# Performance work log

Measured on AMD Instinct MI355X. Metric: run time of the kernel, lower is better.

## Reference

```python
import jax, jax.numpy as jnp
import numpy as np

G = 512  # number of graphs per batch


def gcn_conv(x, edge_index, edge_attr, W):
    # x:[N,Fin], edge_index:[2,E], edge_attr:[E,1], W:[Fin,Fout]
    n = x.shape[0]
    loop = jnp.arange(n)
    row = jnp.concatenate([edge_index[0], loop])
    col = jnp.concatenate([edge_index[1], loop])
    w = jnp.concatenate([edge_attr[:, 0], jnp.ones((n,), x.dtype)])
    deg = jnp.zeros((n,), x.dtype).at[col].add(jnp.ones_like(w))
    dinv = jnp.clip(deg, 1e-12) ** -0.5
    norm = dinv[row] * w * dinv[col]
    h = x @ W  # [N,Fout]
    msg = h[row] * norm[:, None]  # [E+N,Fout] gather+scale
    return jnp.zeros_like(h).at[col].add(msg)  # scatter-add


def mean_pool(x, batch):
    s = jnp.zeros((G, x.shape[1]), x.dtype).at[batch].add(x)
    c = jnp.zeros((G,), x.dtype).at[batch].add(1.0)
    return s / jnp.clip(c, 1.0)[:, None]


def setup_inputs() -> dict:
    key = jax.random.key(0)
    ks = jax.random.split(key, 32)
    Nd, Ed, Np, Ep = 100000, 500000, 200000, 2000000
    d = {
        "drug_x": jax.random.normal(ks[0], (Nd, 78), jnp.float32),
        "drug_edge_index": jax.random.randint(ks[1], (2, Ed), 0, Nd),
        "drug_edge_attr": jax.random.uniform(ks[2], (Ed, 1), jnp.float32),
        "drug_batch": jnp.sort(jax.random.randint(ks[3], (Nd,), 0, G)),
        "protein_x": jax.random.normal(ks[4], (Np, 20), jnp.float32),
        "protein_edge_index": jax.random.randint(ks[5], (2, Ep), 0, Np),
        "protein_edge_attr": jax.random.uniform(ks[6], (Ep, 1), jnp.float32),
        "protein_batch": jnp.sort(jax.random.randint(ks[7], (Np,), 0, G)),
    }
    def w(k, i, o):
        return jax.random.normal(k, (i, o), jnp.float32) / np.sqrt(i)
    d.update({
        "dW1": w(ks[8], 78, 78), "dW2": w(ks[9], 78, 156), "dW3": w(ks[10], 156, 312),
        "dL1_w": w(ks[11], 312, 1024), "dL1_b": jnp.zeros((1024,), jnp.float32),
        "dL2_w": w(ks[12], 1024, 64), "dL2_b": jnp.zeros((64,), jnp.float32),
        "pW1": w(ks[13], 20, 20), "pW2": w(ks[14], 20, 40), "pW3": w(ks[15], 40, 80),
        "pL1_w": w(ks[16], 80, 1024), "pL1_b": jnp.zeros((1024,), jnp.float32),
        "pL2_w": w(ks[17], 1024, 64), "pL2_b": jnp.zeros((64,), jnp.float32),
        "fW1": w(ks[18], 128, 1024), "fb1": jnp.zeros((1024,), jnp.float32),
        "fW2": w(ks[19], 1024, 512), "fb2": jnp.zeros((512,), jnp.float32),
        "fW3": w(ks[20], 512, 1), "fb3": jnp.zeros((1,), jnp.float32),
    })
    return d


def reference(drug_x, drug_edge_index, drug_edge_attr, drug_batch,
              protein_x, protein_edge_index, protein_edge_attr, protein_batch,
              dW1, dW2, dW3, dL1_w, dL1_b, dL2_w, dL2_b,
              pW1, pW2, pW3, pL1_w, pL1_b, pL2_w, pL2_b,
              fW1, fb1, fW2, fb2, fW3, fb3):
    relu = jax.nn.relu
    x = relu(gcn_conv(drug_x, drug_edge_index, drug_edge_attr, dW1))
    x = relu(gcn_conv(x, drug_edge_index, drug_edge_attr, dW2))
    x = relu(gcn_conv(x, drug_edge_index, drug_edge_attr, dW3))
    x = mean_pool(x, drug_batch)
    x = relu(x @ dL1_w + dL1_b)
    x = relu(x @ dL2_w + dL2_b)
    p = relu(gcn_conv(protein_x, protein_edge_index, protein_edge_attr, pW1))
    p = relu(gcn_conv(p, protein_edge_index, protein_edge_attr, pW2))
    p = relu(gcn_conv(p, protein_edge_index, protein_edge_attr, pW3))
    p = mean_pool(p, protein_batch)
    p = relu(p @ pL1_w + pL1_b)
    p = relu(p @ pL2_w + pL2_b)
    c = jnp.concatenate([x, p], axis=1)  # [G,128]
    h = relu(c @ fW1 + fb1)
    h = relu(h @ fW2 + fb2)
    out = h @ fW3 + fb3  # [G,1]
    return out[:, 0]
```

## Files before the change

### kernel.cpp

```cpp
#include <hip/hip_runtime.h>
#include <math.h>

#define NGRAPH 512

typedef __attribute__((ext_vector_type(8))) __bf16 bf16x8;
typedef __attribute__((ext_vector_type(4))) float f32x4;

__device__ __forceinline__ unsigned short f2bf(float x) {
    unsigned int u = __float_as_uint(x);
    u = (u + 0x7fffu + ((u >> 16) & 1u)) >> 16;
    return (unsigned short)u;
}
__device__ __forceinline__ float bf2f(unsigned short b) {
    return __uint_as_float(((unsigned int)b) << 16);
}

static inline unsigned grid_for(size_t n, int block = 256) {
    return (unsigned)((n + block - 1) / block);
}

__global__ void fill_i32(int* __restrict__ p, int v, size_t n) {
    size_t i = blockIdx.x * (size_t)blockDim.x + threadIdx.x;
    if (i < n) p[i] = v;
}

__global__ void hist_kernel(const int* __restrict__ col, int E, int* __restrict__ cnt) {
    size_t i = blockIdx.x * (size_t)blockDim.x + threadIdx.x;
    if (i < (size_t)E) atomicAdd(&cnt[col[i]], 1);
}

__global__ void wcvt(const float* __restrict__ in, unsigned short* __restrict__ out, int n) {
    int i = blockIdx.x * blockDim.x + threadIdx.x;
    if (i < n) out[i] = f2bf(in[i]);
}

__global__ void scan_pass1(const int* __restrict__ in, int* __restrict__ bsum,
                           float* __restrict__ dinv, int n) {
    __shared__ int sdata[256];
    int tid = threadIdx.x;
    int i = blockIdx.x * 256 + tid;
    int v = (i < n) ? in[i] : 0;
    if (i < n) dinv[i] = 1.0f / sqrtf((float)v + 1.0f);
    sdata[tid] = v;
    __syncthreads();
    for (int s = 128; s > 0; s >>= 1) {
        if (tid < s) sdata[tid] += sdata[tid + s];
        __syncthreads();
    }
    if (tid == 0) bsum[blockIdx.x] = sdata[0];
}

__global__ void scan_pass2(int* __restrict__ bsum, int nb) {
    __shared__ int s[1024];
    int tid = threadIdx.x;
    int v = (tid < nb) ? bsum[tid] : 0;
    s[tid] = v;
    __syncthreads();
    for (int ofs = 1; ofs < 1024; ofs <<= 1) {
        int t = (tid >= ofs) ? s[tid - ofs] : 0;
        __syncthreads();
        s[tid] += t;
        __syncthreads();
    }
    if (tid < nb) bsum[tid] = s[tid] - v;
}

__global__ void scan_pass3(int* __restrict__ pos, const int* __restrict__ bsum, int n) {
    __shared__ int sdata[256];
    int tid = threadIdx.x;
    int i = blockIdx.x * 256 + tid;
    int v = (i < n) ? pos[i] : 0;
    sdata[tid] = v;
    __syncthreads();
    for (int ofs = 1; ofs < 256; ofs <<= 1) {
        int t = (tid >= ofs) ? sdata[tid - ofs] : 0;
        __syncthreads();
        sdata[tid] += t;
        __syncthreads();
    }
    if (i < n) pos[i] = sdata[tid] - v + bsum[blockIdx.x];
}

__global__ void csr_fill(const int* __restrict__ row, const int* __restrict__ col,
                         const float* __restrict__ attr, const float* __restrict__ dinv,
                         int* __restrict__ pos, int* __restrict__ rowp,
                         float* __restrict__ coefp, int E) {
    size_t i = blockIdx.x * (size_t)blockDim.x + threadIdx.x;
    if (i >= (size_t)E) return;
    int r = row[i], c = col[i];
    int slot = atomicAdd(&pos[c], 1);
    rowp[slot] = r;
    coefp[slot] = dinv[r] * attr[i] * dinv[c];
}

template <int V, int LPG, int F, int LDI, int LDO, bool INBF>
__global__ void gather_bf(const int* __restrict__ pos, const int* __restrict__ rowp,
                          const float* __restrict__ coefp, const void* __restrict__ Xv,
                          const float* __restrict__ dinv, unsigned short* __restrict__ AGG,
                          int N) {
    constexpr int gpb = 256 / LPG;
    int grp = threadIdx.x / LPG;
    if (grp >= gpb) return;
    int gid = blockIdx.x * gpb + grp;
    int lane = threadIdx.x - grp * LPG;
    if (gid >= N) return;

    auto load_row = [&](int r, float* dst) {
        if (INBF) {
            const unsigned short* X = (const unsigned short*)Xv;
            if (V == 2) {
                unsigned int u = *reinterpret_cast<const unsigned int*>(X + (size_t)r * LDI + lane * 2);
                dst[0] = bf2f((unsigned short)(u & 0xffffu));
                dst[1] = bf2f((unsigned short)(u >> 16));
            } else {
                uint2 u = *reinterpret_cast<const uint2*>(X + (size_t)r * LDI + lane * 4);
                dst[0] = bf2f((unsigned short)(u.x & 0xffffu));
                dst[1] = bf2f((unsigned short)(u.x >> 16));
                dst[2] = bf2f((unsigned short)(u.y & 0xffffu));
                dst[3] = bf2f((unsigned short)(u.y >> 16));
            }
        } else {
            const float* X = (const float*)Xv;
            if (V == 2) {
                float2 u = *reinterpret_cast<const float2*>(X + (size_t)r * LDI + lane * 2);
                dst[0] = u.x; dst[1] = u.y;
            } else {
                float4 u = *reinterpret_cast<const float4*>(X + (size_t)r * LDI + lane * 4);
                dst[0] = u.x; dst[1] = u.y; dst[2] = u.z; dst[3] = u.w;
            }
        }
    };

    int start = (gid == 0) ? 0 : pos[gid - 1];
    int end = pos[gid];
    float s = dinv[gid];
    float s2 = s * s;
    float acc[V];
    load_row(gid, acc);
#pragma unroll
    for (int j = 0; j < V; ++j) acc[j] *= s2;
    int t = start;
    for (; t + 4 <= end; t += 4) {
        int r0 = rowp[t], r1 = rowp[t + 1], r2 = rowp[t + 2], r3 = rowp[t + 3];
        float c0 = coefp[t], c1 = coefp[t + 1], c2 = coefp[t + 2], c3 = coefp[t + 3];
        float h0[V], h1[V], h2[V], h3[V];
        load_row(r0, h0); load_row(r1, h1); load_row(r2, h2); load_row(r3, h3);
#pragma unroll
        for (int j = 0; j < V; ++j) {
            float v = fmaf(c0, h0[j], acc[j]);
            v = fmaf(c1, h1[j], v);
            v = fmaf(c2, h2[j], v);
            acc[j] = fmaf(c3, h3[j], v);
        }
    }
    for (; t < end; ++t) {
        int r = rowp[t];
        float cf = coefp[t];
        float h[V];
        load_row(r, h);
#pragma unroll
        for (int j = 0; j < V; ++j) acc[j] = fmaf(cf, h[j], acc[j]);
    }
    unsigned short* op = AGG + (size_t)gid * LDO + lane * V;
    if (V == 2) {
        unsigned int p = (unsigned int)f2bf(acc[0]) | ((unsigned int)f2bf(acc[1]) << 16);
        *reinterpret_cast<unsigned int*>(op) = p;
    } else {
        uint2 p;
        p.x = (unsigned int)f2bf(acc[0]) | ((unsigned int)f2bf(acc[1]) << 16);
        p.y = (unsigned int)f2bf(acc[2]) | ((unsigned int)f2bf(acc[3]) << 16);
        *reinterpret_cast<uint2*>(op) = p;
    }
    constexpr int PAD = LDO - F;
#pragma unroll
    for (int p = lane; p < PAD; p += LPG) AGG[(size_t)gid * LDO + F + p] = 0;
}

template <int KPAD, int BN>
__global__ __launch_bounds__(256) void tgemm_mfma(
        const unsigned short* __restrict__ A, const unsigned short* __restrict__ Wb,
        unsigned short* __restrict__ C, int M, int K, int N, int ldc) {
    constexpr int LDT = KPAD + 8;
    constexpr int KSTEPS = KPAD / 32;
    constexpr int NI = (BN / 2) / 16;
    __shared__ unsigned short As[128 * LDT];
    __shared__ unsigned short Bs[BN * LDT];
    const int tid = threadIdx.x;
    const int m0 = blockIdx.y * 128;
    const int n0 = blockIdx.x * BN;

    for (int idx = tid; idx < 128 * (KPAD / 4); idx += 256) {
        int m = idx / (KPAD / 4);
        int kc = idx - m * (KPAD / 4);
        int gm = m0 + m;
        uint2 v = make_uint2(0u, 0u);
        if (gm < M) v = *reinterpret_cast<const uint2*>(A + (size_t)gm * KPAD + kc * 4);
        *reinterpret_cast<uint2*>(&As[m * LDT + kc * 4]) = v;
    }
    for (int idx = tid; idx < BN * KPAD; idx += 256) {
        int k = idx / BN;
        int n = idx - k * BN;
        int gn = n0 + n;
        unsigned short v = 0;
        if (k < K && gn < N) v = Wb[(size_t)k * N + gn];
        Bs[n * LDT + k] = v;
    }
    __syncthreads();

    const int wid = tid >> 6;
    const int l = tid & 63;
    const int wm = wid >> 1, wn = wid & 1;
    const int lr = l & 15, lg = l >> 4;

    f32x4 acc[4][NI];
#pragma unroll
    for (int i = 0; i < 4; ++i)
#pragma unroll
        for (int j = 0; j < NI; ++j) acc[i][j] = (f32x4){0.f, 0.f, 0.f, 0.f};

    for (int ks = 0; ks < KSTEPS; ++ks) {
        bf16x8 a[4], b[NI];
#pragma unroll
        for (int mi = 0; mi < 4; ++mi)
            a[mi] = *reinterpret_cast<const bf16x8*>(
                &As[(wm * 64 + mi * 16 + lr) * LDT + ks * 32 + lg * 8]);
#pragma unroll
        for (int ni = 0; ni < NI; ++ni)
            b[ni] = *reinterpret_cast<const bf16x8*>(
                &Bs[(wn * (BN / 2) + ni * 16 + lr) * LDT + ks * 32 + lg * 8]);
#pragma unroll
        for (int mi = 0; mi < 4; ++mi)
#pragma unroll
            for (int ni = 0; ni < NI; ++ni)
                acc[mi][ni] = __builtin_amdgcn_mfma_f32_16x16x32_bf16(
                    a[mi], b[ni], acc[mi][ni], 0, 0, 0);
    }

#pragma unroll
    for (int mi = 0; mi < 4; ++mi) {
#pragma unroll
        for (int ni = 0; ni < NI; ++ni) {
#pragma unroll
            for (int j = 0; j < 4; ++j) {
                int gm = m0 + wm * 64 + mi * 16 + lg * 4 + j;
                int gn = n0 + wn * (BN / 2) + ni * 16 + lr;
                if (gm < M && gn < N)
                    C[(size_t)gm * ldc + gn] = f2bf(fmaxf(acc[mi][ni][j], 0.0f));
            }
        }
    }
}

__global__ void pool_mean_bf(const unsigned short* __restrict__ X, const int* __restrict__ batch,
                             float* __restrict__ out, int N, int F) {
    int g = blockIdx.x;
    int lo = 0, hi = N;
    while (lo < hi) { int mid = (lo + hi) >> 1; if (batch[mid] < g) lo = mid + 1; else hi = mid; }
    int s0 = lo;
    hi = N;
    while (lo < hi) { int mid = (lo + hi) >> 1; if (batch[mid] < g + 1) lo = mid + 1; else hi = mid; }
    int s1 = lo;
    int c = s1 - s0;
    float inv = 1.0f / (float)(c > 0 ? c : 1);
    for (int f = threadIdx.x; f < F; f += blockDim.x) {
        float acc = 0.0f;
        for (int n = s0; n < s1; ++n) acc += fmaxf(bf2f(X[(size_t)n * F + f]), 0.0f);
        out[(size_t)g * F + f] = acc * inv;
    }
}

template <int K, int NOUT>
__global__ __launch_bounds__(64 * (K / 4)) void fused_conv(
        const int* __restrict__ pos, const int* __restrict__ rowp,
        const float* __restrict__ coefp, const float* __restrict__ X,
        const float* __restrict__ dinv, const float* __restrict__ W,
        float* __restrict__ Y, int N) {
    constexpr int LPG = K / 4;
    constexpr int NTHREADS = 64 * LPG;
    union U { float4 v; float a[4]; };
    __shared__ float Ws[K][NOUT];
    __shared__ float Ag[64][K + 4];
    const int tid = threadIdx.x;
    const int nid0 = blockIdx.x * 64;

    for (int i = tid; i < K * NOUT; i += NTHREADS) Ws[i / NOUT][i % NOUT] = W[i];

    int grp = tid / LPG, lane = tid % LPG;
    int gid = nid0 + grp;
    if (gid < N) {
        int start = (gid == 0) ? 0 : pos[gid - 1];
        int end = pos[gid];
        float s = dinv[gid];
        float s2 = s * s;
        U acc;
        acc.v = *reinterpret_cast<const float4*>(X + (size_t)gid * K + lane * 4);
#pragma unroll
        for (int j = 0; j < 4; ++j) acc.a[j] *= s2;
        int t = start;
        for (; t + 4 <= end; t += 4) {
            int r0 = rowp[t], r1 = rowp[t + 1], r2 = rowp[t + 2], r3 = rowp[t + 3];
            float c0 = coefp[t], c1 = coefp[t + 1], c2 = coefp[t + 2], c3 = coefp[t + 3];
            U h0, h1, h2, h3;
            h0.v = *reinterpret_cast<const float4*>(X + (size_t)r0 * K + lane * 4);
            h1.v = *reinterpret_cast<const float4*>(X + (size_t)r1 * K + lane * 4);
            h2.v = *reinterpret_cast<const float4*>(X + (size_t)r2 * K + lane * 4);
            h3.v = *reinterpret_cast<const float4*>(X + (size_t)r3 * K + lane * 4);
#pragma unroll
            for (int j = 0; j < 4; ++j) {
                float v = fmaf(c0, h0.a[j], acc.a[j]);
                v = fmaf(c1, h1.a[j], v);
                v = fmaf(c2, h2.a[j], v);
                acc.a[j] = fmaf(c3, h3.a[j], v);
            }
        }
        for (; t < end; ++t) {
            int r = rowp[t];
            float cf = coefp[t];
            U h;
            h.v = *reinterpret_cast<const float4*>(X + (size_t)r * K + lane * 4);
#pragma unroll
            for (int j = 0; j < 4; ++j) acc.a[j] = fmaf(cf, h.a[j], acc.a[j]);
        }
        *reinterpret_cast<float4*>(&Ag[grp][lane * 4]) = acc.v;
    }
    __syncthreads();

    for (int idx = tid; idx < 64 * NOUT; idx += NTHREADS) {
        int nl = idx / NOUT, n = idx % NOUT;
        int g = nid0 + nl;
        if (g < N) {
            float acc = 0.0f;
#pragma unroll
            for (int k = 0; k < K; ++k) acc = fmaf(Ag[nl][k], Ws[k][n], acc);
            Y[(size_t)g * NOUT + n] = fmaxf(acc, 0.0f);
        }
    }
}

__global__ void pool_mean_s(const float* __restrict__ X, const int* __restrict__ batch,
                            float* __restrict__ out, int N, int F, int S) {
    __shared__ float red[256];
    int g = blockIdx.x;
    int lo = 0, hi = N;
    while (lo < hi) { int mid = (lo + hi) >> 1; if (batch[mid] < g) lo = mid + 1; else hi = mid; }
    int s0 = lo;
    hi = N;
    while (lo < hi) { int mid = (lo + hi) >> 1; if (batch[mid] < g + 1) lo = mid + 1; else hi = mid; }
    int s1 = lo;
    int c = s1 - s0;
    float inv = 1.0f / (float)(c > 0 ? c : 1);
    int t = threadIdx.x;
    int stripe = t / F;
    int f = t - stripe * F;
    float acc = 0.0f;
    if (stripe < S) {
        for (int n = s0 + stripe; n < s1; n += S)
            acc += fmaxf(X[(size_t)n * F + f], 0.0f);
    }
    red[t] = acc;
    __syncthreads();
    if (t < F) {
        float v = red[t];
        for (int s = 1; s < S; ++s) v += red[t + s * F];
        out[(size_t)g * F + t] = v * inv;
    }
}

template <bool RELU_OUT>
__global__ __launch_bounds__(256) void skinny_gemm4(
        const float* __restrict__ A, const float* __restrict__ W,
        const float* __restrict__ bias, float* __restrict__ C,
        int K, int M, int ldc, int coff) {
    __shared__ float As[4][1024];
    __shared__ float red[4][64][4];
    const int tid = threadIdx.x;
    const int m_l = tid & 63;
    const int q = tid >> 6;
    const int g0 = blockIdx.y * 4;
    const int m0 = blockIdx.x * 64;

    for (int idx = tid; idx < 4 * K; idx += 256)
        As[idx / K][idx % K] = A[(size_t)(g0 + idx / K) * K + idx % K];
    __syncthreads();

    const int Kq = (K + 3) >> 2;
    const int ks = q * Kq;
    const int ke = (ks + Kq < K) ? ks + Kq : K;
    const int m = m0 + m_l;
    float acc[4] = {0.0f, 0.0f, 0.0f, 0.0f};
    if (m < M) {
        for (int k = ks; k < ke; ++k) {
            float w = W[(size_t)k * M + m];
            acc[0] = fmaf(As[0][k], w, acc[0]);
            acc[1] = fmaf(As[1][k], w, acc[1]);
            acc[2] = fmaf(As[2][k], w, acc[2]);
            acc[3] = fmaf(As[3][k], w, acc[3]);
        }
    }
#pragma unroll
    for (int g = 0; g < 4; ++g) red[q][m_l][g] = acc[g];
    __syncthreads();
    if (q == 0 && m < M) {
        float b = bias[m];
#pragma unroll
        for (int g = 0; g < 4; ++g) {
            float v = red[0][m_l][g] + red[1][m_l][g] + red[2][m_l][g] + red[3][m_l][g] + b;
            if (RELU_OUT) v = fmaxf(v, 0.0f);
            C[(size_t)(g0 + g) * ldc + coff + m] = v;
        }
    }
}

__global__ void final_kernel(const float* __restrict__ A, const float* __restrict__ w,
                             const float* __restrict__ b, float* __restrict__ out, int K) {
    int wave = (blockIdx.x * blockDim.x + threadIdx.x) >> 6;
    int lane = threadIdx.x & 63;
    if (wave >= NGRAPH) return;
    const float* ar = A + (size_t)wave * K;
    float acc = 0.0f;
    for (int k = lane; k < K; k += 64) acc = fmaf(ar[k], w[k], acc);
#pragma unroll
    for (int s = 32; s > 0; s >>= 1) acc += __shfl_down(acc, s, 64);
    if (lane == 0) out[wave] = acc + b[0];
}

static void build_csr(const int* row, const int* col, const float* attr,
                      int N, int E, float* dinv, int* pos,
                      int* rowp, float* coefp, int* bsum, hipStream_t stream) {
    const int B = 256;
    int nb = (N + 255) / 256;
    fill_i32<<<grid_for(N), B, 0, stream>>>(pos, 0, (size_t)N);
    hist_kernel<<<grid_for(E), B, 0, stream>>>(col, E, pos);
    scan_pass1<<<nb, B, 0, stream>>>(pos, bsum, dinv, N);
    scan_pass2<<<1, 1024, 0, stream>>>(bsum, nb);
    scan_pass3<<<nb, B, 0, stream>>>(pos, bsum, N);
    csr_fill<<<grid_for(E), B, 0, stream>>>(row, col, attr, dinv, pos, rowp, coefp, E);
}

extern "C" void kernel_launch(void* const* d_in, const int* in_sizes, int n_in,
                              void* d_out, int out_size, void* d_ws, size_t ws_size,
                              hipStream_t stream) {
    const float* drug_x  = (const float*)d_in[0];
    const int*   d_ei    = (const int*)d_in[1];
    const float* d_ea    = (const float*)d_in[2];
    const int*   d_batch = (const int*)d_in[3];
    const float* prot_x  = (const float*)d_in[4];
    const int*   p_ei    = (const int*)d_in[5];
    const float* p_ea    = (const float*)d_in[6];
    const int*   p_batch = (const int*)d_in[7];
    const float* dW1 = (const float*)d_in[8];
    const float* dW2 = (const float*)d_in[9];
    const float* dW3 = (const float*)d_in[10];
    const float* dL1_w = (const float*)d_in[11];
    const float* dL1_b = (const float*)d_in[12];
    const float* dL2_w = (const float*)d_in[13];
    const float* dL2_b = (const float*)d_in[14];
    const float* pW1 = (const float*)d_in[15];
    const float* pW2 = (const float*)d_in[16];
    const float* pW3 = (const float*)d_in[17];
    const float* pL1_w = (const float*)d_in[18];
    const float* pL1_b = (const float*)d_in[19];
    const float* pL2_w = (const float*)d_in[20];
    const float* pL2_b = (const float*)d_in[21];
    const float* fW1 = (const float*)d_in[22];
    const float* fb1 = (const float*)d_in[23];
    const float* fW2 = (const float*)d_in[24];
    const float* fb2 = (const float*)d_in[25];
    const float* fW3 = (const float*)d_in[26];
    const float* fb3 = (const float*)d_in[27];
    float* out = (float*)d_out;

    const int Nd = in_sizes[0] / 78;
    const int Ed = in_sizes[1] / 2;
    const int Np = in_sizes[4] / 20;
    const int Ep = in_sizes[5] / 2;
    const int* d_row = d_ei;
    const int* d_col = d_ei + Ed;
    const int* p_row = p_ei;
    const int* p_col = p_ei + Ep;

    float* ws = (float*)d_ws;
    size_t off = 0;
    auto align256 = [](size_t n) -> size_t { return (n + 255) & ~(size_t)255; };
    auto take = [&](size_t n) -> float* {
        float* p = ws + off;
        off += align256(n);
        return p;
    };
    float* B1      = take((size_t)Nd * 312);
    float* B2      = take((size_t)Nd * 312);
    float* dinv_d  = take((size_t)Nd);
    float* dinv_p  = take((size_t)Np);
    float* pool    = take((size_t)NGRAPH * 312);
    float* t1      = take((size_t)NGRAPH * 1024);
    float* Cbuf    = take((size_t)NGRAPH * 128);
    float* f2buf   = take((size_t)NGRAPH * 512);
    int*   bsum    = (int*)take(1056);
    int*   pos_d   = (int*)take((size_t)Nd);
    int*   rowp_d  = (int*)take((size_t)Ed);
    float* coefp_d = take((size_t)Ed);
    unsigned short* Wb1 = (unsigned short*)take((78 * 78 + 1) / 2);
    unsigned short* Wb2 = (unsigned short*)take((78 * 156 + 1) / 2);
    unsigned short* Wb3 = (unsigned short*)take((156 * 312 + 1) / 2);
    size_t tail = align256((size_t)Np * 80);
    int*   pos_p   = (int*)(B1 + tail);
    int*   rowp_p  = (int*)(B1 + tail + align256((size_t)Np));
    float* coefp_p = B1 + tail + align256((size_t)Np) + align256((size_t)Ep);
    (void)ws_size;

    unsigned short* B1u = (unsigned short*)B1;
    unsigned short* B2u = (unsigned short*)B2;

    const int B = 256;
    auto gblocks = [](int n, int gpb) -> unsigned { return (unsigned)((n + gpb - 1) / gpb); };
    auto mgrid = [](int M, int N, int BN) -> dim3 {
        return dim3((unsigned)((N + BN - 1) / BN), (unsigned)((M + 127) / 128));
    };

    build_csr(d_row, d_col, d_ea, Nd, Ed, dinv_d, pos_d, rowp_d, coefp_d, bsum, stream);
    wcvt<<<grid_for(78 * 78), B, 0, stream>>>(dW1, Wb1, 78 * 78);
    wcvt<<<grid_for(78 * 156), B, 0, stream>>>(dW2, Wb2, 78 * 156);
    wcvt<<<grid_for(156 * 312), B, 0, stream>>>(dW3, Wb3, 156 * 312);

    gather_bf<2, 39, 78, 78, 96, false><<<gblocks(Nd, 256 / 39), B, 0, stream>>>(
        pos_d, rowp_d, coefp_d, drug_x, dinv_d, B2u, Nd);
    tgemm_mfma<96, 64><<<mgrid(Nd, 78, 64), B, 0, stream>>>(B2u, Wb1, B1u, Nd, 78, 78, 80);

    gather_bf<2, 39, 78, 80, 96, true><<<gblocks(Nd, 256 / 39), B, 0, stream>>>(
        pos_d, rowp_d, coefp_d, B1u, dinv_d, B2u, Nd);
    tgemm_mfma<96, 64><<<mgrid(Nd, 156, 64), B, 0, stream>>>(B2u, Wb2, B1u, Nd, 78, 156, 156);

    gather_bf<4, 39, 156, 156, 160, true><<<gblocks(Nd, 256 / 39), B, 0, stream>>>(
        pos_d, rowp_d, coefp_d, B1u, dinv_d, B2u, Nd);
    tgemm_mfma<160, 64><<<mgrid(Nd, 312, 64), B, 0, stream>>>(B2u, Wb3, B1u, Nd, 156, 312, 312);

    pool_mean_bf<<<NGRAPH, B, 0, stream>>>(B1u, d_batch, pool, Nd, 312);

    skinny_gemm4<true><<<dim3(16, NGRAPH / 4), B, 0, stream>>>(pool, dL1_w, dL1_b, t1, 312, 1024, 1024, 0);
    skinny_gemm4<true><<<dim3(1, NGRAPH / 4), B, 0, stream>>>(t1, dL2_w, dL2_b, Cbuf, 1024, 64, 128, 0);

    build_csr(p_row, p_col, p_ea, Np, Ep, dinv_p, pos_p, rowp_p, coefp_p, bsum, stream);

    fused_conv<20, 20><<<gblocks(Np, 64), 320, 0, stream>>>(
        pos_p, rowp_p, coefp_p, prot_x, dinv_p, pW1, B1, Np);
    fused_conv<20, 40><<<gblocks(Np, 64), 320, 0, stream>>>(
        pos_p, rowp_p, coefp_p, B1, dinv_p, pW2, B2, Np);
    fused_conv<40, 80><<<gblocks(Np, 64), 640, 0, stream>>>(
        pos_p, rowp_p, coefp_p, B2, dinv_p, pW3, B1, Np);

    pool_mean_s<<<NGRAPH, B, 0, stream>>>(B1, p_batch, pool, Np, 80, 3);

    skinny_gemm4<true><<<dim3(16, NGRAPH / 4), B, 0, stream>>>(pool, pL1_w, pL1_b, t1, 80, 1024, 1024, 0);
    skinny_gemm4<true><<<dim3(1, NGRAPH / 4), B, 0, stream>>>(t1, pL2_w, pL2_b, Cbuf, 1024, 64, 128, 64);

    skinny_gemm4<true><<<dim3(16, NGRAPH / 4), B, 0, stream>>>(Cbuf, fW1, fb1, t1, 128, 1024, 1024, 0);
    skinny_gemm4<true><<<dim3(8, NGRAPH / 4), B, 0, stream>>>(t1, fW2, fb2, f2buf, 1024, 512, 512, 0);
    final_kernel<<<grid_for((size_t)NGRAPH * 64), B, 0, stream>>>(f2buf, fW3, fb3, out, 512);
}
```

Before: 1.247 ms.

## Pack CSR row/coef into int2, pre-transpose bf16 weights, swizzle GEMM LDS tiles

CSR edges now store row index and coefficient together as one int2, so each edge costs a single 8-byte load instead of two separate loads. Weights are converted into a transposed, K-padded bf16 layout, which lets the MFMA GEMM read B fragments straight from global memory/L2 instead of staging them in LDS. The A tile is stored with an XOR swizzle instead of padding. The trade-offs are a larger K padding (96→128, 160→192), which raises gather write traffic and MFMA work, and B loads that now go through global memory.

```diff
diff --git a/kernel.cpp b/kernel.cpp
--- a/kernel.cpp
+++ b/kernel.cpp
@@ -29,9 +29,12 @@
     if (i < (size_t)E) atomicAdd(&cnt[col[i]], 1);
 }
 
-__global__ void wcvt(const float* __restrict__ in, unsigned short* __restrict__ out, int n) {
+__global__ void wcvt_t(const float* __restrict__ in, unsigned short* __restrict__ out,
+                       int K, int N, int KPAD) {
     int i = blockIdx.x * blockDim.x + threadIdx.x;
-    if (i < n) out[i] = f2bf(in[i]);
+    if (i >= N * KPAD) return;
+    int n = i / KPAD, k = i - n * KPAD;
+    out[i] = (k < K) ? f2bf(in[(size_t)k * N + n]) : (unsigned short)0;
 }
 
 __global__ void scan_pass1(const int* __restrict__ in, int* __restrict__ bsum,
@@ -83,21 +86,18 @@
 
 __global__ void csr_fill(const int* __restrict__ row, const int* __restrict__ col,
                          const float* __restrict__ attr, const float* __restrict__ dinv,
-                         int* __restrict__ pos, int* __restrict__ rowp,
-                         float* __restrict__ coefp, int E) {
+                         int* __restrict__ pos, int2* __restrict__ rcp, int E) {
     size_t i = blockIdx.x * (size_t)blockDim.x + threadIdx.x;
     if (i >= (size_t)E) return;
     int r = row[i], c = col[i];
     int slot = atomicAdd(&pos[c], 1);
-    rowp[slot] = r;
-    coefp[slot] = dinv[r] * attr[i] * dinv[c];
+    rcp[slot] = make_int2(r, __float_as_int(dinv[r] * attr[i] * dinv[c]));
 }
 
 template <int V, int LPG, int F, int LDI, int LDO, bool INBF>
-__global__ void gather_bf(const int* __restrict__ pos, const int* __restrict__ rowp,
-                          const float* __restrict__ coefp, const void* __restrict__ Xv,
-                          const float* __restrict__ dinv, unsigned short* __restrict__ AGG,
-                          int N) {
+__global__ void gather_bf(const int* __restrict__ pos, const int2* __restrict__ rcp,
+                          const void* __restrict__ Xv, const float* __restrict__ dinv,
+                          unsigned short* __restrict__ AGG, int N) {
     constexpr int gpb = 256 / LPG;
     int grp = threadIdx.x / LPG;
     if (grp >= gpb) return;
@@ -141,10 +141,11 @@
     for (int j = 0; j < V; ++j) acc[j] *= s2;
     int t = start;
     for (; t + 4 <= end; t += 4) {
-        int r0 = rowp[t], r1 = rowp[t + 1], r2 = rowp[t + 2], r3 = rowp[t + 3];
-        float c0 = coefp[t], c1 = coefp[t + 1], c2 = coefp[t + 2], c3 = coefp[t + 3];
+        int2 e0 = rcp[t], e1 = rcp[t + 1], e2 = rcp[t + 2], e3 = rcp[t + 3];
+        float c0 = __int_as_float(e0.y), c1 = __int_as_float(e1.y);
+        float c2 = __int_as_float(e2.y), c3 = __int_as_float(e3.y);
         float h0[V], h1[V], h2[V], h3[V];
-        load_row(r0, h0); load_row(r1, h1); load_row(r2, h2); load_row(r3, h3);
+        load_row(e0.x, h0); load_row(e1.x, h1); load_row(e2.x, h2); load_row(e3.x, h3);
 #pragma unroll
         for (int j = 0; j < V; ++j) {
             float v = fmaf(c0, h0[j], acc[j]);
@@ -154,10 +155,10 @@
         }
     }
     for (; t < end; ++t) {
-        int r = rowp[t];
-        float cf = coefp[t];
+        int2 e = rcp[t];
+        float cf = __int_as_float(e.y);
         float h[V];
-        load_row(r, h);
+        load_row(e.x, h);
 #pragma unroll
         for (int j = 0; j < V; ++j) acc[j] = fmaf(cf, h[j], acc[j]);
     }
@@ -178,32 +179,24 @@
 
 template <int KPAD, int BN>
 __global__ __launch_bounds__(256) void tgemm_mfma(
-        const unsigned short* __restrict__ A, const unsigned short* __restrict__ Wb,
-        unsigned short* __restrict__ C, int M, int K, int N, int ldc) {
-    constexpr int LDT = KPAD + 8;
+        const unsigned short* __restrict__ A, const unsigned short* __restrict__ Wt,
+        unsigned short* __restrict__ C, int M, int N, int ldc) {
+    constexpr int CH = KPAD / 8;
     constexpr int KSTEPS = KPAD / 32;
     constexpr int NI = (BN / 2) / 16;
-    __shared__ unsigned short As[128 * LDT];
-    __shared__ unsigned short Bs[BN * LDT];
+    __shared__ unsigned short As[128 * KPAD];
     const int tid = threadIdx.x;
     const int m0 = blockIdx.y * 128;
     const int n0 = blockIdx.x * BN;
 
-    for (int idx = tid; idx < 128 * (KPAD / 4); idx += 256) {
-        int m = idx / (KPAD / 4);
-        int kc = idx - m * (KPAD / 4);
+    for (int idx = tid; idx < 128 * CH; idx += 256) {
+        int m = idx / CH;
+        int c = idx - m * CH;
         int gm = m0 + m;
-        uint2 v = make_uint2(0u, 0u);
-        if (gm < M) v = *reinterpret_cast<const uint2*>(A + (size_t)gm * KPAD + kc * 4);
-        *reinterpret_cast<uint2*>(&As[m * LDT + kc * 4]) = v;
-    }
-    for (int idx = tid; idx < BN * KPAD; idx += 256) {
-        int k = idx / BN;
-        int n = idx - k * BN;
-        int gn = n0 + n;
-        unsigned short v = 0;
-        if (k < K && gn < N) v = Wb[(size_t)k * N + gn];
-        Bs[n * LDT + k] = v;
+        uint4 v = make_uint4(0u, 0u, 0u, 0u);
+        if (gm < M) v = *reinterpret_cast<const uint4*>(A + (size_t)gm * KPAD + c * 8);
+        int cs = c ^ (m & 7);
+        *reinterpret_cast<uint4*>(&As[m * KPAD + cs * 8]) = v;
     }
     __syncthreads();
 
@@ -221,13 +214,18 @@
     for (int ks = 0; ks < KSTEPS; ++ks) {
         bf16x8 a[4], b[NI];
 #pragma unroll
-        for (int mi = 0; mi < 4; ++mi)
-            a[mi] = *reinterpret_cast<const bf16x8*>(
-                &As[(wm * 64 + mi * 16 + lr) * LDT + ks * 32 + lg * 8]);
-#pragma unroll
-        for (int ni = 0; ni < NI; ++ni)
+        for (int mi = 0; mi < 4; ++mi) {
+            int row = wm * 64 + mi * 16 + lr;
+            int cs = (ks * 4 + lg) ^ (row & 7);
+            a[mi] = *reinterpret_cast<const bf16x8*>(&As[row * KPAD + cs * 8]);
+        }
+#pragma unroll
+        for (int ni = 0; ni < NI; ++ni) {
+            int gn = n0 + wn * (BN / 2) + ni * 16 + lr;
+            int gns = (gn < N) ? gn : (N - 1);
             b[ni] = *reinterpret_cast<const bf16x8*>(
-                &Bs[(wn * (BN / 2) + ni * 16 + lr) * LDT + ks * 32 + lg * 8]);
+                &Wt[(size_t)gns * KPAD + ks * 32 + lg * 8]);
+        }
 #pragma unroll
         for (int mi = 0; mi < 4; ++mi)
 #pragma unroll
@@ -271,10 +269,9 @@
 
 template <int K, int NOUT>
 __global__ __launch_bounds__(64 * (K / 4)) void fused_conv(
-        const int* __restrict__ pos, const int* __restrict__ rowp,
-        const float* __restrict__ coefp, const float* __restrict__ X,
-        const float* __restrict__ dinv, const float* __restrict__ W,
-        float* __restrict__ Y, int N) {
+        const int* __restrict__ pos, const int2* __restrict__ rcp,
+        const float* __restrict__ X, const float* __restrict__ dinv,
+        const float* __restrict__ W, float* __restrict__ Y, int N) {
     constexpr int LPG = K / 4;
     constexpr int NTHREADS = 64 * LPG;
     union U { float4 v; float a[4]; };
@@ -298,13 +295,14 @@
         for (int j = 0; j < 4; ++j) acc.a[j] *= s2;
         int t = start;
         for (; t + 4 <= end; t += 4) {
-            int r0 = rowp[t], r1 = rowp[t + 1], r2 = rowp[t + 2], r3 = rowp[t + 3];
-            float c0 = coefp[t], c1 = coefp[t + 1], c2 = coefp[t + 2], c3 = coefp[t + 3];
+            int2 e0 = rcp[t], e1 = rcp[t + 1], e2 = rcp[t + 2], e3 = rcp[t + 3];
+            float c0 = __int_as_float(e0.y), c1 = __int_as_float(e1.y);
+            float c2 = __int_as_float(e2.y), c3 = __int_as_float(e3.y);
             U h0, h1, h2, h3;
-            h0.v = *reinterpret_cast<const float4*>(X + (size_t)r0 * K + lane * 4);
-            h1.v = *reinterpret_cast<const float4*>(X + (size_t)r1 * K + lane * 4);
-            h2.v = *reinterpret_cast<const float4*>(X + (size_t)r2 * K + lane * 4);
-            h3.v = *reinterpret_cast<const float4*>(X + (size_t)r3 * K + lane * 4);
+            h0.v = *reinterpret_cast<const float4*>(X + (size_t)e0.x * K + lane * 4);
+            h1.v = *reinterpret_cast<const float4*>(X + (size_t)e1.x * K + lane * 4);
+            h2.v = *reinterpret_cast<const float4*>(X + (size_t)e2.x * K + lane * 4);
+            h3.v = *reinterpret_cast<const float4*>(X + (size_t)e3.x * K + lane * 4);
 #pragma unroll
             for (int j = 0; j < 4; ++j) {
                 float v = fmaf(c0, h0.a[j], acc.a[j]);
@@ -314,10 +312,10 @@
             }
         }
         for (; t < end; ++t) {
-            int r = rowp[t];
-            float cf = coefp[t];
+            int2 e = rcp[t];
+            float cf = __int_as_float(e.y);
             U h;
-            h.v = *reinterpret_cast<const float4*>(X + (size_t)r * K + lane * 4);
+            h.v = *reinterpret_cast<const float4*>(X + (size_t)e.x * K + lane * 4);
 #pragma unroll
             for (int j = 0; j < 4; ++j) acc.a[j] = fmaf(cf, h.a[j], acc.a[j]);
         }
@@ -426,7 +424,7 @@
 
 static void build_csr(const int* row, const int* col, const float* attr,
                       int N, int E, float* dinv, int* pos,
-                      int* rowp, float* coefp, int* bsum, hipStream_t stream) {
+                      int2* rcp, int* bsum, hipStream_t stream) {
     const int B = 256;
     int nb = (N + 255) / 256;
     fill_i32<<<grid_for(N), B, 0, stream>>>(pos, 0, (size_t)N);
@@ -434,7 +432,7 @@
     scan_pass1<<<nb, B, 0, stream>>>(pos, bsum, dinv, N);
     scan_pass2<<<1, 1024, 0, stream>>>(bsum, nb);
     scan_pass3<<<nb, B, 0, stream>>>(pos, bsum, N);
-    csr_fill<<<grid_for(E), B, 0, stream>>>(row, col, attr, dinv, pos, rowp, coefp, E);
+    csr_fill<<<grid_for(E), B, 0, stream>>>(row, col, attr, dinv, pos, rcp, E);
 }
 
 extern "C" void kernel_launch(void* const* d_in, const int* in_sizes, int n_in,
@@ -497,15 +495,13 @@
     float* f2buf   = take((size_t)NGRAPH * 512);
     int*   bsum    = (int*)take(1056);
     int*   pos_d   = (int*)take((size_t)Nd);
-    int*   rowp_d  = (int*)take((size_t)Ed);
-    float* coefp_d = take((size_t)Ed);
-    unsigned short* Wb1 = (unsigned short*)take((78 * 78 + 1) / 2);
-    unsigned short* Wb2 = (unsigned short*)take((78 * 156 + 1) / 2);
-    unsigned short* Wb3 = (unsigned short*)take((156 * 312 + 1) / 2);
+    int2*  rcp_d   = (int2*)take((size_t)Ed * 2);
+    unsigned short* Wt1 = (unsigned short*)take((78 * 128) / 2);
+    unsigned short* Wt2 = (unsigned short*)take((156 * 128) / 2);
+    unsigned short* Wt3 = (unsigned short*)take((312 * 192) / 2);
     size_t tail = align256((size_t)Np * 80);
     int*   pos_p   = (int*)(B1 + tail);
-    int*   rowp_p  = (int*)(B1 + tail + align256((size_t)Np));
-    float* coefp_p = B1 + tail + align256((size_t)Np) + align256((size_t)Ep);
+    int2*  rcp_p   = (int2*)(B1 + tail + align256((size_t)Np));
     (void)ws_size;
 
     unsigned short* B1u = (unsigned short*)B1;
@@ -517,36 +513,36 @@
         return dim3((unsigned)((N + BN - 1) / BN), (unsigned)((M + 127) / 128));
     };
 
-    build_csr(d_row, d_col, d_ea, Nd, Ed, dinv_d, pos_d, rowp_d, coefp_d, bsum, stream);
-    wcvt<<<grid_for(78 * 78), B, 0, stream>>>(dW1, Wb1, 78 * 78);
-    wcvt<<<grid_for(78 * 156), B, 0, stream>>>(dW2, Wb2, 78 * 156);
-    wcvt<<<grid_for(156 * 312), B, 0, stream>>>(dW3, Wb3, 156 * 312);
-
-    gather_bf<2, 39, 78, 78, 96, false><<<gblocks(Nd, 256 / 39), B, 0, stream>>>(
-        pos_d, rowp_d, coefp_d, drug_x, dinv_d, B2u, Nd);
-    tgemm_mfma<96, 64><<<mgrid(Nd, 78, 64), B, 0, stream>>>(B2u, Wb1, B1u, Nd, 78, 78, 80);
-
-    gather_bf<2, 39, 78, 80, 96, true><<<gblocks(Nd, 256 / 39), B, 0, stream>>>(
-        pos_d, rowp_d, coefp_d, B1u, dinv_d, B2u, Nd);
-    tgemm_mfma<96, 64><<<mgrid(Nd, 156, 64), B, 0, stream>>>(B2u, Wb2, B1u, Nd, 78, 156, 156);
-
-    gather_bf<4, 39, 156, 156, 160, true><<<gblocks(Nd, 256 / 39), B, 0, stream>>>(
-        pos_d, rowp_d, coefp_d, B1u, dinv_d, B2u, Nd);
-    tgemm_mfma<160, 64><<<mgrid(Nd, 312, 64), B, 0, stream>>>(B2u, Wb3, B1u, Nd, 156, 312, 312);
+    build_csr(d_row, d_col, d_ea, Nd, Ed, dinv_d, pos_d, rcp_d, bsum, stream);
+    wcvt_t<<<grid_for(78 * 128), B, 0, stream>>>(dW1, Wt1, 78, 78, 128);
+    wcvt_t<<<grid_for(156 * 128), B, 0, stream>>>(dW2, Wt2, 78, 156, 128);
+    wcvt_t<<<grid_for(312 * 192), B, 0, stream>>>(dW3, Wt3, 156, 312, 192);
+
+    gather_bf<2, 39, 78, 78, 128, false><<<gblocks(Nd, 256 / 39), B, 0, stream>>>(
+        pos_d, rcp_d, drug_x, dinv_d, B2u, Nd);
+    tgemm_mfma<128, 64><<<mgrid(Nd, 78, 64), B, 0, stream>>>(B2u, Wt1, B1u, Nd, 78, 80);
+
+    gather_bf<2, 39, 78, 80, 128, true><<<gblocks(Nd, 256 / 39), B, 0, stream>>>(
+        pos_d, rcp_d, B1u, dinv_d, B2u, Nd);
+    tgemm_mfma<128, 64><<<mgrid(Nd, 156, 64), B, 0, stream>>>(B2u, Wt2, B1u, Nd, 156, 156);
+
+    gather_bf<4, 39, 156, 156, 192, true><<<gblocks(Nd, 256 / 39), B, 0, stream>>>(
+        pos_d, rcp_d, B1u, dinv_d, B2u, Nd);
+    tgemm_mfma<192, 64><<<mgrid(Nd, 312, 64), B, 0, stream>>>(B2u, Wt3, B1u, Nd, 312, 312);
 
     pool_mean_bf<<<NGRAPH, B, 0, stream>>>(B1u, d_batch, pool, Nd, 312);
 
     skinny_gemm4<true><<<dim3(16, NGRAPH / 4), B, 0, stream>>>(pool, dL1_w, dL1_b, t1, 312, 1024, 1024, 0);
     skinny_gemm4<true><<<dim3(1, NGRAPH / 4), B, 0, stream>>>(t1, dL2_w, dL2_b, Cbuf, 1024, 64, 128, 0);
 
-    build_csr(p_row, p_col, p_ea, Np, Ep, dinv_p, pos_p, rowp_p, coefp_p, bsum, stream);
+    build_csr(p_row, p_col, p_ea, Np, Ep, dinv_p, pos_p, rcp_p, bsum, stream);
 
     fused_conv<20, 20><<<gblocks(Np, 64), 320, 0, stream>>>(
-        pos_p, rowp_p, coefp_p, prot_x, dinv_p, pW1, B1, Np);
+        pos_p, rcp_p, prot_x, dinv_p, pW1, B1, Np);
     fused_conv<20, 40><<<gblocks(Np, 64), 320, 0, stream>>>(
-        pos_p, rowp_p, coefp_p, B1, dinv_p, pW2, B2, Np);
+        pos_p, rcp_p, B1, dinv_p, pW2, B2, Np);
     fused_conv<40, 80><<<gblocks(Np, 64), 640, 0, stream>>>(
-        pos_p, rowp_p, coefp_p, B2, dinv_p, pW3, B1, Np);
+        pos_p, rcp_p, B2, dinv_p, pW3, B1, Np);
 
     pool_mean_s<<<NGRAPH, B, 0, stream>>>(B1, p_batch, pool, Np, 80, 3);
 
```

Result: faster. 1.111 ms (-10.9%).
